# Performance work log

Measured on AMD Instinct MI355X. Metric: run time of the kernel, lower is better.

Reference implementation:

```python
import jax, jax.numpy as jnp
import numpy as np

B, NBAND, C, T = 2, 40, 64, 1500
NUM_CODE = 1024


def setup_inputs() -> dict:
    key = jax.random.key(0)
    k1, k2 = jax.random.split(key)
    x = jax.random.normal(k1, (B, NBAND, C, T), dtype=jnp.float32)
    # layer_idx == 0 init: unit-norm codes per band
    cb = jax.random.normal(k2, (NBAND, NUM_CODE, C), dtype=jnp.float32)
    eps = jnp.finfo(jnp.float32).eps
    cb = cb / jnp.sqrt(jnp.sum(cb * cb, axis=-1, keepdims=True) + eps)
    return {"x": x, "codebook": cb}


def reference(x, codebook):
    batch, nband, nchan, time = x.shape
    num_code = codebook.shape[1]
    # x.detach().permute(0,3,1,2).view(B*T, nband, nchan)
    xd = jax.lax.stop_gradient(x).transpose(0, 3, 1, 2).reshape(batch * time, nband, nchan)
    dist = (
        jnp.sum(xd * xd, axis=-1, keepdims=True)
        + jnp.sum(codebook * codebook, axis=-1)
        - 2.0 * jnp.einsum("nbc,bkc->nbk", xd, codebook)
    )
    min_idx = jnp.argmin(dist, axis=-1)  # [BT, nband]
    # per-band gather: quantized[n, b] = codebook[b, min_idx[n, b]]
    quantized = codebook[jnp.arange(nband)[None, :], min_idx]  # [BT, nband, nchan]
    # view(B, T, nband, nchan).permute(0,2,3,1)
    return quantized.reshape(batch, time, nband, nchan).transpose(0, 2, 3, 1)
```

## Files before the change

kernel.cpp:

```cpp
#include <hip/hip_runtime.h>


#define NBAND  40
#define CH     64
#define TT     1500
#define NCODE  1024
#define MT     128
#define NTILE  12
#define PAD    68
#define THRESH 1e-3f

typedef short v8s __attribute__((ext_vector_type(8)));
typedef float v4f __attribute__((ext_vector_type(4)));

#define CBF_USHORTS ((size_t)NBAND * 32 * 8 * 64 * 8)
#define CBF_BYTES   (CBF_USHORTS * 2)
#define WS_NEEDED   (CBF_BYTES + (size_t)NBAND * NCODE * 4)

__device__ __forceinline__ unsigned short f2bf(float f) {
    unsigned u = __float_as_uint(f);
    return (unsigned short)((u + 0x7FFFu + ((u >> 16) & 1u)) >> 16);
}
__device__ __forceinline__ float bf2f(unsigned short h) {
    return __uint_as_float(((unsigned)h) << 16);
}
__device__ __forceinline__ unsigned ford(float f) {
    unsigned u = __float_as_uint(f);
    return (u & 0x80000000u) ? ~u : (u | 0x80000000u);
}
__device__ __forceinline__ float finv(unsigned u) {
    return (u & 0x80000000u) ? __uint_as_float(u & 0x7FFFFFFFu) : __uint_as_float(~u);
}
__device__ __forceinline__ unsigned long long packsk(float f, unsigned k) {
    return ((unsigned long long)ford(f) << 32) | (unsigned long long)k;
}
__device__ __forceinline__ float med3f(float a, float b, float c) {
#if __has_builtin(__builtin_amdgcn_fmed3f)
    return __builtin_amdgcn_fmed3f(a, b, c);
#else
    return fminf(fmaxf(a, b), c);
#endif
}

typedef __attribute__((address_space(1))) const unsigned char* gas_p;
typedef __attribute__((address_space(3))) unsigned char*       las_p;
__device__ __forceinline__ void async_ld16(const void* g, void* l) {
    __builtin_amdgcn_global_load_lds((gas_p)g, (las_p)l, 16, 0, 0);
}

__global__ __launch_bounds__(256)
void vq_prep(const float* __restrict__ cb,
             unsigned short* __restrict__ CBF,
             float* __restrict__ C2) {
    const int id     = blockIdx.x;
    const int v      = id >> 3;
    const int band   = (id & 7) + 8 * (v % 5);
    const int gchunk = v / 5;
    const int g      = gchunk * 4 + (threadIdx.x >> 6);
    const int lane   = threadIdx.x & 63;
    const int col    = lane & 15;
    const int quad   = lane >> 4;

    float sq[2] = {0.f, 0.f};
    #pragma unroll
    for (int l = 0; l < 4; ++l) {
        const int ni = l >> 1, ks = l & 1;
        const int code = g * 32 + ni * 16 + col;
        const int c0   = ks * 32 + quad * 8;
        const float* src = cb + ((size_t)(band * NCODE + code)) * CH + c0;
        const float4 v0 = *(const float4*)src;
        const float4 v1 = *(const float4*)(src + 4);
        const float vv[8] = {v0.x, v0.y, v0.z, v0.w, v1.x, v1.y, v1.z, v1.w};
        union { unsigned short u[8]; v8s v; } hh, ll;
        #pragma unroll
        for (int j = 0; j < 8; ++j) {
            const unsigned short h = f2bf(vv[j]);
            hh.u[j] = h;
            ll.u[j] = f2bf(vv[j] - bf2f(h));
            sq[ni] = fmaf(vv[j], vv[j], sq[ni]);
        }
        const size_t gb = (size_t)(band * 32 + g) * 8;
        *(v8s*)&CBF[(gb + l)     * 512 + lane * 8] = hh.v;
        *(v8s*)&CBF[(gb + 4 + l) * 512 + lane * 8] = ll.v;
    }
    #pragma unroll
    for (int ni = 0; ni < 2; ++ni) {
        sq[ni] += __shfl_xor(sq[ni], 16);
        sq[ni] += __shfl_xor(sq[ni], 32);
    }
    if (quad == 0) {
        C2[band * NCODE + g * 32 + col]      = sq[0];
        C2[band * NCODE + g * 32 + 16 + col] = sq[1];
    }
}

__global__ __launch_bounds__(256, 3)
void vq_main(const float* __restrict__ x,
             const float* __restrict__ cb,
             const unsigned short* __restrict__ CBF,
             const float* __restrict__ C2f,
             float* __restrict__ out) {
    __shared__ alignas(16) unsigned char SMEM[MT * PAD * 2 * 2];
    __shared__ float c2_s[NCODE];
    __shared__ unsigned long long best_s[MT];
    __shared__ unsigned long long MB_s[MT * 2];
    __shared__ float MS_s[MT * 2];
    __shared__ unsigned amb_s[4];
    __shared__ float xrow_s[CH];

    const int id    = blockIdx.x;
    const int v     = id >> 3;
    const int band  = (id & 7) + 8 * (v % 5);
    const int tb    = v / 5;
    const int tile  = tb % NTILE;
    const int batch = tb / NTILE;
    const int t0    = tile * MT;

    const int tid   = threadIdx.x;
    const int wave  = tid >> 6;
    const int lane  = tid & 63;
    const int quad  = lane >> 4;
    const int col   = lane & 15;
    const int thalf = wave & 1;
    const int khalf = wave >> 1;

    if (tid < 4) amb_s[tid] = 0u;
    {
        const float* src = C2f + band * NCODE;
        #pragma unroll
        for (int i = 0; i < 4; ++i) c2_s[tid + 256 * i] = src[tid + 256 * i];
    }
    {
        unsigned short* XH_s = (unsigned short*)SMEM;
        unsigned short* XL_s = XH_s + MT * PAD;
        const int c = tid & 63;
        const int g = tid >> 6;
        const float* src = x + ((size_t)(batch * NBAND + band) * CH + c) * TT + t0;
        #pragma unroll
        for (int i = 0; i < 8; ++i) {
            const int t = (g + 4 * i) * 4;
            float4 v4 = make_float4(0.f, 0.f, 0.f, 0.f);
            if (t0 + t + 3 < TT) v4 = *(const float4*)(src + t);
            const float vv[4] = {v4.x, v4.y, v4.z, v4.w};
            #pragma unroll
            for (int j = 0; j < 4; ++j) {
                const unsigned short h = f2bf(vv[j]);
                XH_s[(t + j) * PAD + c] = h;
                XL_s[(t + j) * PAD + c] = f2bf(vv[j] - bf2f(h));
            }
        }
    }
    __syncthreads();

    v8s ah[4][2], al[4][2];
    {
        unsigned short* XH_s = (unsigned short*)SMEM;
        unsigned short* XL_s = XH_s + MT * PAD;
        #pragma unroll
        for (int mi = 0; mi < 4; ++mi)
            #pragma unroll
            for (int ks = 0; ks < 2; ++ks) {
                const int off = (thalf * 64 + mi * 16 + col) * PAD + ks * 32 + quad * 8;
                ah[mi][ks] = *(const v8s*)&XH_s[off];
                al[mi][ks] = *(const v8s*)&XL_s[off];
            }
    }
    __syncthreads();

    float m1[16], m2[16];
    int   id16[16];
    #pragma unroll
    for (int i = 0; i < 16; ++i) { m1[i] = 3.4028235e38f; m2[i] = 3.4028235e38f; id16[i] = 0x7fffffff; }

    unsigned short* LBUF = (unsigned short*)SMEM;
    const unsigned short* cbase = CBF + (size_t)(band * 32) * 4096 + (size_t)lane * 8;
    const int pbase = thalf * 4;

    auto stage_round = [&](int r, int b) {
        const int group = khalf * 16 + r;
        #pragma unroll
        for (int i = 0; i < 4; ++i) {
            const int p = pbase + i;
            async_ld16(cbase + (size_t)group * 4096 + p * 512,
                       LBUF + (size_t)b * 8192 + khalf * 4096 + p * 512);
        }
    };

    stage_round(0, 0);

    for (int r = 0; r < 16; ++r) {
        __syncthreads();
        if (r + 1 < 16) stage_round(r + 1, (r + 1) & 1);

        const unsigned short* lb = LBUF + (size_t)(r & 1) * 8192 + khalf * 4096 + lane * 8;
        #pragma unroll
        for (int ni = 0; ni < 2; ++ni) {
            v4f acc[4];
            #pragma unroll
            for (int mi = 0; mi < 4; ++mi) acc[mi] = (v4f){0.f, 0.f, 0.f, 0.f};
            #pragma unroll
            for (int ks = 0; ks < 2; ++ks) {
                const v8s bh = *(const v8s*)(lb + (ni * 2 + ks) * 512);
                #pragma unroll
                for (int mi = 0; mi < 4; ++mi)
                    acc[mi] = __builtin_amdgcn_mfma_f32_16x16x32_bf16(ah[mi][ks], bh, acc[mi], 0, 0, 0);
                #pragma unroll
                for (int mi = 0; mi < 4; ++mi)
                    acc[mi] = __builtin_amdgcn_mfma_f32_16x16x32_bf16(al[mi][ks], bh, acc[mi], 0, 0, 0);
                const v8s bl = *(const v8s*)(lb + (4 + ni * 2 + ks) * 512);
                #pragma unroll
                for (int mi = 0; mi < 4; ++mi)
                    acc[mi] = __builtin_amdgcn_mfma_f32_16x16x32_bf16(ah[mi][ks], bl, acc[mi], 0, 0, 0);
            }
            const int   kg  = khalf * 512 + r * 32 + ni * 16 + col;
            const float c2v = c2_s[kg];
            #pragma unroll
            for (int mi = 0; mi < 4; ++mi)
                #pragma unroll
                for (int rr = 0; rr < 4; ++rr) {
                    const int j = mi * 4 + rr;
                    const float s = fmaf(-2.f, acc[mi][rr], c2v);
                    m2[j] = med3f(s, m1[j], m2[j]);
                    const bool lt = s < m1[j];
                    m1[j]   = lt ? s : m1[j];
                    id16[j] = lt ? kg : id16[j];
                }
        }
    }

    #pragma unroll
    for (int j = 0; j < 16; ++j) {
        float b1 = m1[j], b2 = m2[j];
        int   bi = id16[j];
        #pragma unroll
        for (int d = 1; d < 16; d <<= 1) {
            const float o1 = __shfl_xor(b1, d);
            const float o2 = __shfl_xor(b2, d);
            const int   oi = __shfl_xor(bi, d);
            b2 = fminf(fminf(b2, o2), fmaxf(b1, o1));
            const bool take = (o1 < b1) || (o1 == b1 && oi < bi);
            b1 = take ? o1 : b1;
            bi = take ? oi : bi;
        }
        if (col == 0) {
            const int t = thalf * 64 + (j >> 2) * 16 + quad * 4 + (j & 3);
            MB_s[t * 2 + khalf] = packsk(b1, (unsigned)bi);
            MS_s[t * 2 + khalf] = b2;
        }
    }
    __syncthreads();

    if (tid < MT) {
        const unsigned long long b0 = MB_s[tid * 2];
        const unsigned long long b1 = MB_s[tid * 2 + 1];
        const unsigned long long bmin = (b0 < b1) ? b0 : b1;
        const unsigned long long bmax = (b0 < b1) ? b1 : b0;
        const float M1 = finv((unsigned)(bmin >> 32));
        const float M2 = fminf(fminf(MS_s[tid * 2], MS_s[tid * 2 + 1]), finv((unsigned)(bmax >> 32)));
        best_s[tid] = bmin;
        if ((M2 - M1) <= THRESH && t0 + tid < TT)
            atomicOr(&amb_s[tid >> 5], 1u << (tid & 31));
    }
    __syncthreads();

    for (int t = 0; t < MT; ++t) {
        if ((amb_s[t >> 5] >> (t & 31)) & 1u) {
            if (tid < CH) xrow_s[tid] = x[((size_t)(batch * NBAND + band) * CH + tid) * TT + t0 + t];
            if (tid == CH) best_s[t] = ~0ULL;
            __syncthreads();
            #pragma unroll
            for (int i = 0; i < 4; ++i) {
                const int k = tid * 4 + i;
                const float* crow = cb + ((size_t)(band * NCODE + k)) * CH;
                float dot = 0.f, c2e = 0.f;
                #pragma unroll 8
                for (int c = 0; c < CH; ++c) {
                    const float cv = crow[c];
                    dot = fmaf(cv, xrow_s[c], dot);
                    c2e = fmaf(cv, cv, c2e);
                }
                atomicMin(&best_s[t], packsk(fmaf(-2.f, dot, c2e), (unsigned)k));
            }
            __syncthreads();
        }
    }
    __syncthreads();

    {
        float* OT = (float*)SMEM;
        #pragma unroll
        for (int rr = 0; rr < MT; rr += 4) {
            const int row = rr + wave;
            const unsigned idx = (unsigned)(best_s[row] & 0xFFFFFFFFull) & (NCODE - 1);
            OT[row * 67 + lane] = cb[((size_t)(band * NCODE + idx)) * CH + lane];
        }
        __syncthreads();
        const int tloc  = tid & 127;
        const int chalf = tid >> 7;
        if (t0 + tloc < TT) {
            float* ob = out + ((size_t)(batch * NBAND + band) * CH) * TT + t0 + tloc;
            #pragma unroll
            for (int i = 0; i < 32; ++i) {
                const int c = chalf * 32 + i;
                ob[(size_t)c * TT] = OT[tloc * 67 + c];
            }
        }
    }
}

#define TN 128
#define KC 128
__global__ __launch_bounds__(256, 2)
void vq_fp32_kernel(const float* __restrict__ x,
                    const float* __restrict__ cb,
                    float* __restrict__ out) {
    __shared__ float XT_s[CH * TN];
    __shared__ float CBT_s[CH * KC];
    __shared__ float c2part[256];
    const int tile = blockIdx.x, band = blockIdx.y, batch = blockIdx.z;
    const int t0 = tile * TN;
    const int tid = threadIdx.x;
    const int tx = tid & 15, ty = tid >> 4;
    {
        const int c = tid >> 2, q = tid & 3;
        const float* src = x + ((size_t)(batch * NBAND + band) * CH + c) * TT + t0;
        #pragma unroll
        for (int i = 0; i < 8; ++i) {
            const int t = q * 32 + i * 4;
            float4 v = make_float4(0.f, 0.f, 0.f, 0.f);
            if (t0 + t < TT) v = *(const float4*)(src + t);
            *(float4*)&XT_s[c * TN + t] = v;
        }
    }
    float vmin[8]; int vidx[8];
    #pragma unroll
    for (int i = 0; i < 8; ++i) { vmin[i] = 3.4e38f; vidx[i] = 0x7fffffff; }
    for (int kc = 0; kc < NCODE; kc += KC) {
        __syncthreads();
        {
            const int k = tid >> 1, ch0 = (tid & 1) * 32;
            const float* src = cb + ((size_t)(band * NCODE + kc + k)) * CH + ch0;
            float s = 0.f;
            #pragma unroll
            for (int i = 0; i < 8; ++i) {
                const float4 v = *(const float4*)(src + i * 4);
                const int c0 = ch0 + i * 4;
                CBT_s[(c0 + 0) * KC + k] = v.x; CBT_s[(c0 + 1) * KC + k] = v.y;
                CBT_s[(c0 + 2) * KC + k] = v.z; CBT_s[(c0 + 3) * KC + k] = v.w;
                s = fmaf(v.x, v.x, s); s = fmaf(v.y, v.y, s);
                s = fmaf(v.z, v.z, s); s = fmaf(v.w, v.w, s);
            }
            c2part[tid] = s;
        }
        __syncthreads();
        float acc[8][8];
        #pragma unroll
        for (int ii = 0; ii < 8; ++ii)
            #pragma unroll
            for (int jj = 0; jj < 8; ++jj) acc[ii][jj] = 0.f;
        #pragma unroll 4
        for (int c = 0; c < CH; ++c) {
            const float4 xa0 = *(const float4*)&XT_s[c * TN + tx * 4];
            const float4 xa1 = *(const float4*)&XT_s[c * TN + 64 + tx * 4];
            const float4 cv0 = *(const float4*)&CBT_s[c * KC + ty * 4];
            const float4 cv1 = *(const float4*)&CBT_s[c * KC + 64 + ty * 4];
            const float xa[8] = {xa0.x, xa0.y, xa0.z, xa0.w, xa1.x, xa1.y, xa1.z, xa1.w};
            const float cv[8] = {cv0.x, cv0.y, cv0.z, cv0.w, cv1.x, cv1.y, cv1.z, cv1.w};
            #pragma unroll
            for (int ii = 0; ii < 8; ++ii)
                #pragma unroll
                for (int jj = 0; jj < 8; ++jj) acc[ii][jj] = fmaf(xa[ii], cv[jj], acc[ii][jj]);
        }
        #pragma unroll
        for (int jj = 0; jj < 8; ++jj) {
            const int kl = (jj < 4) ? (ty * 4 + jj) : (64 + ty * 4 + (jj - 4));
            const float c2v = c2part[2 * kl] + c2part[2 * kl + 1];
            const int kglob = kc + kl;
            #pragma unroll
            for (int ii = 0; ii < 8; ++ii) {
                const float score = fmaf(-2.f, acc[ii][jj], c2v);
                if (score < vmin[ii]) { vmin[ii] = score; vidx[ii] = kglob; }
            }
        }
    }
    __syncthreads();
    float* redv = XT_s;
    int* redi = (int*)(XT_s + TN * 16);
    int* idxs = (int*)(XT_s + TN * 32);
    #pragma unroll
    for (int ii = 0; ii < 8; ++ii) {
        const int t = (ii < 4) ? (tx * 4 + ii) : (64 + tx * 4 + (ii - 4));
        redv[t * 16 + ty] = vmin[ii];
        redi[t * 16 + ty] = vidx[ii];
    }
    __syncthreads();
    if (tid < TN) {
        float bv = redv[tid * 16]; int bi = redi[tid * 16];
        #pragma unroll
        for (int j = 1; j < 16; ++j) {
            const float v = redv[tid * 16 + j]; const int id = redi[tid * 16 + j];
            if (v < bv || (v == bv && id < bi)) { bv = v; bi = id; }
        }
        idxs[tid] = bi;
    }
    __syncthreads();
    {
        const int tloc = tid & 127, chalf = tid >> 7;
        if (t0 + tloc < TT) {
            const int idx = idxs[tloc];
            const float* crow = cb + ((size_t)(band * NCODE + idx)) * CH;
            float* ob = out + ((size_t)(batch * NBAND + band) * CH) * TT + t0 + tloc;
            #pragma unroll
            for (int i = 0; i < 32; ++i) {
                const int c = chalf * 32 + i;
                ob[(size_t)c * TT] = crow[c];
            }
        }
    }
}

extern "C" void kernel_launch(void* const* d_in, const int* in_sizes, int n_in,
                              void* d_out, int out_size, void* d_ws, size_t ws_size,
                              hipStream_t stream) {
    const float* x  = (const float*)d_in[0];
    const float* cb = (const float*)d_in[1];
    float* out = (float*)d_out;
    if (ws_size >= WS_NEEDED) {
        unsigned short* CBF = (unsigned short*)d_ws;
        float* C2 = (float*)((char*)d_ws + CBF_BYTES);
        vq_prep<<<dim3(8 * 5 * 8), dim3(256), 0, stream>>>(cb, CBF, C2);
        vq_main<<<dim3(8 * 5 * NTILE * 2), dim3(256), 0, stream>>>(x, cb, CBF, C2, out);
    } else {
        dim3 grid((TT + TN - 1) / TN, NBAND, 2);
        vq_fp32_kernel<<<grid, dim3(256), 0, stream>>>(x, cb, out);
    }
}
```

Measured before the change: 215.7 us.

## Split VQ search into x-prep, k-sliced partial argmin, and merge kernels

Replaces the monolithic per-tile kernel with four kernels. x is pre-split into bf16 hi/lo MFMA fragments in workspace. A k-sliced partial kernel launches 8x more blocks, each scanning 128 codes with smaller register and LDS footprint, and writes per-slice best and second-best scores. A merge kernel reduces the slices, runs the fp32 refinement for ambiguous rows and gathers the output. This is meant to raise parallelism and occupancy, at the cost of extra launches, workspace round trips and a strided x read in the prep kernel.

```diff
diff --git a/kernel.cpp b/kernel.cpp
--- a/kernel.cpp
+++ b/kernel.cpp
@@ -7,15 +7,22 @@
 #define NCODE  1024
 #define MT     128
 #define NTILE  12
-#define PAD    68
+#define NTG    48
 #define THRESH 1e-3f
 
 typedef short v8s __attribute__((ext_vector_type(8)));
 typedef float v4f __attribute__((ext_vector_type(4)));
 
-#define CBF_USHORTS ((size_t)NBAND * 32 * 8 * 64 * 8)
-#define CBF_BYTES   (CBF_USHORTS * 2)
-#define WS_NEEDED   (CBF_BYTES + (size_t)NBAND * NCODE * 4)
+#define CBF_BYTES  ((size_t)NBAND * 32 * 8 * 64 * 8 * 2)
+#define XF_OFF     CBF_BYTES
+#define XF_BYTES   ((size_t)2 * NBAND * NTG * 8 * 64 * 8 * 2)
+#define C2_OFF     (XF_OFF + XF_BYTES)
+#define C2_BYTES   ((size_t)NBAND * NCODE * 4)
+#define PB_OFF     (C2_OFF + C2_BYTES)
+#define PB_BYTES   ((size_t)2 * NBAND * 8 * 1536 * 8)
+#define PS_OFF     (PB_OFF + PB_BYTES)
+#define PS_BYTES   (PB_BYTES / 2)
+#define WS_NEEDED  (PS_OFF + PS_BYTES)
 
 __device__ __forceinline__ unsigned short f2bf(float f) {
     unsigned u = __float_as_uint(f);
@@ -49,9 +56,9 @@
 }
 
 __global__ __launch_bounds__(256)
-void vq_prep(const float* __restrict__ cb,
-             unsigned short* __restrict__ CBF,
-             float* __restrict__ C2) {
+void vq_prep_cb(const float* __restrict__ cb,
+                unsigned short* __restrict__ CBF,
+                float* __restrict__ C2) {
     const int id     = blockIdx.x;
     const int v      = id >> 3;
     const int band   = (id & 7) + 8 * (v % 5);
@@ -94,144 +101,137 @@
     }
 }
 
-__global__ __launch_bounds__(256, 3)
-void vq_main(const float* __restrict__ x,
-             const float* __restrict__ cb,
-             const unsigned short* __restrict__ CBF,
-             const float* __restrict__ C2f,
-             float* __restrict__ out) {
-    __shared__ alignas(16) unsigned char SMEM[MT * PAD * 2 * 2];
-    __shared__ float c2_s[NCODE];
-    __shared__ unsigned long long best_s[MT];
-    __shared__ unsigned long long MB_s[MT * 2];
-    __shared__ float MS_s[MT * 2];
-    __shared__ unsigned amb_s[4];
-    __shared__ float xrow_s[CH];
-
+__global__ __launch_bounds__(256)
+void vq_prep_x(const float* __restrict__ x,
+               unsigned short* __restrict__ XF) {
     const int id    = blockIdx.x;
     const int v     = id >> 3;
     const int band  = (id & 7) + 8 * (v % 5);
-    const int tb    = v / 5;
-    const int tile  = tb % NTILE;
-    const int batch = tb / NTILE;
-    const int t0    = tile * MT;
-
-    const int tid   = threadIdx.x;
-    const int wave  = tid >> 6;
-    const int lane  = tid & 63;
-    const int quad  = lane >> 4;
-    const int col   = lane & 15;
-    const int thalf = wave & 1;
-    const int khalf = wave >> 1;
-
-    if (tid < 4) amb_s[tid] = 0u;
+    const int u     = v / 5;
+    const int batch = u & 1;
+    const int chunk = u >> 1;
+    const int bb    = batch * NBAND + band;
+
+    const int wave = threadIdx.x >> 6;
+    const int lane = threadIdx.x & 63;
+    const int quad = lane >> 4;
+    const int col  = lane & 15;
+
+    #pragma unroll
+    for (int i = 0; i < 2; ++i) {
+        const int tg = chunk * 8 + wave * 2 + i;
+        #pragma unroll
+        for (int pp = 0; pp < 4; ++pp) {
+            const int mi = pp >> 1, ks = pp & 1;
+            const int t  = tg * 32 + mi * 16 + col;
+            union { unsigned short u[8]; v8s v; } hh, ll;
+            #pragma unroll
+            for (int j = 0; j < 8; ++j) {
+                const int c = ks * 32 + quad * 8 + j;
+                const float val = (t < TT) ? x[((size_t)bb * CH + c) * TT + t] : 0.f;
+                const unsigned short h = f2bf(val);
+                hh.u[j] = h;
+                ll.u[j] = f2bf(val - bf2f(h));
+            }
+            const size_t base = ((size_t)bb * NTG + tg) * 8;
+            *(v8s*)&XF[(base + pp)     * 512 + lane * 8] = hh.v;
+            *(v8s*)&XF[(base + 4 + pp) * 512 + lane * 8] = ll.v;
+        }
+    }
+}
+
+__global__ __launch_bounds__(256, 4)
+void vq_partial(const unsigned short* __restrict__ XF,
+                const unsigned short* __restrict__ CBF,
+                const float* __restrict__ C2f,
+                unsigned long long* __restrict__ PB,
+                float* __restrict__ PS) {
+    __shared__ alignas(16) unsigned short LBUF[4 * 8 * 512];
+
+    const int id     = blockIdx.x;
+    const int v      = id >> 3;
+    const int band   = (id & 7) + 8 * (v % 5);
+    const int u      = v / 5;
+    const int batch  = u & 1;
+    const int u2     = u >> 1;
+    const int tile   = u2 % NTILE;
+    const int kslice = u2 / NTILE;
+    const int bb     = batch * NBAND + band;
+
+    const int tid  = threadIdx.x;
+    const int wave = tid >> 6;
+    const int lane = tid & 63;
+    const int quad = lane >> 4;
+    const int col  = lane & 15;
+
     {
-        const float* src = C2f + band * NCODE;
-        #pragma unroll
-        for (int i = 0; i < 4; ++i) c2_s[tid + 256 * i] = src[tid + 256 * i];
-    }
+        const unsigned short* cbase =
+            CBF + ((size_t)(band * 32 + kslice * 4) * 8) * 512 + (size_t)lane * 8;
+        #pragma unroll
+        for (int i = 0; i < 8; ++i) {
+            const int fp = wave * 8 + i;
+            async_ld16(cbase + (size_t)fp * 512, LBUF + (size_t)fp * 512 + lane * 8);
+        }
+    }
+    v8s ah[2][2], al[2][2];
     {
-        unsigned short* XH_s = (unsigned short*)SMEM;
-        unsigned short* XL_s = XH_s + MT * PAD;
-        const int c = tid & 63;
-        const int g = tid >> 6;
-        const float* src = x + ((size_t)(batch * NBAND + band) * CH + c) * TT + t0;
-        #pragma unroll
-        for (int i = 0; i < 8; ++i) {
-            const int t = (g + 4 * i) * 4;
-            float4 v4 = make_float4(0.f, 0.f, 0.f, 0.f);
-            if (t0 + t + 3 < TT) v4 = *(const float4*)(src + t);
-            const float vv[4] = {v4.x, v4.y, v4.z, v4.w};
-            #pragma unroll
-            for (int j = 0; j < 4; ++j) {
-                const unsigned short h = f2bf(vv[j]);
-                XH_s[(t + j) * PAD + c] = h;
-                XL_s[(t + j) * PAD + c] = f2bf(vv[j] - bf2f(h));
-            }
-        }
-    }
-    __syncthreads();
-
-    v8s ah[4][2], al[4][2];
-    {
-        unsigned short* XH_s = (unsigned short*)SMEM;
-        unsigned short* XL_s = XH_s + MT * PAD;
-        #pragma unroll
-        for (int mi = 0; mi < 4; ++mi)
+        const int tg = tile * 4 + wave;
+        const unsigned short* xb =
+            XF + (((size_t)bb * NTG + tg) * 8) * 512 + (size_t)lane * 8;
+        #pragma unroll
+        for (int mi = 0; mi < 2; ++mi)
             #pragma unroll
             for (int ks = 0; ks < 2; ++ks) {
-                const int off = (thalf * 64 + mi * 16 + col) * PAD + ks * 32 + quad * 8;
-                ah[mi][ks] = *(const v8s*)&XH_s[off];
-                al[mi][ks] = *(const v8s*)&XL_s[off];
-            }
-    }
-    __syncthreads();
-
-    float m1[16], m2[16];
-    int   id16[16];
-    #pragma unroll
-    for (int i = 0; i < 16; ++i) { m1[i] = 3.4028235e38f; m2[i] = 3.4028235e38f; id16[i] = 0x7fffffff; }
-
-    unsigned short* LBUF = (unsigned short*)SMEM;
-    const unsigned short* cbase = CBF + (size_t)(band * 32) * 4096 + (size_t)lane * 8;
-    const int pbase = thalf * 4;
-
-    auto stage_round = [&](int r, int b) {
-        const int group = khalf * 16 + r;
-        #pragma unroll
-        for (int i = 0; i < 4; ++i) {
-            const int p = pbase + i;
-            async_ld16(cbase + (size_t)group * 4096 + p * 512,
-                       LBUF + (size_t)b * 8192 + khalf * 4096 + p * 512);
-        }
-    };
-
-    stage_round(0, 0);
-
-    for (int r = 0; r < 16; ++r) {
-        __syncthreads();
-        if (r + 1 < 16) stage_round(r + 1, (r + 1) & 1);
-
-        const unsigned short* lb = LBUF + (size_t)(r & 1) * 8192 + khalf * 4096 + lane * 8;
+                ah[mi][ks] = *(const v8s*)(xb + (mi * 2 + ks) * 512);
+                al[mi][ks] = *(const v8s*)(xb + (4 + mi * 2 + ks) * 512);
+            }
+    }
+    __syncthreads();
+
+    float m1[8], m2[8];
+    int   id8[8];
+    #pragma unroll
+    for (int i = 0; i < 8; ++i) { m1[i] = 3.4028235e38f; m2[i] = 3.4028235e38f; id8[i] = 0x7fffffff; }
+
+    #pragma unroll
+    for (int gi = 0; gi < 4; ++gi) {
+        const unsigned short* lb = LBUF + gi * 4096 + lane * 8;
         #pragma unroll
         for (int ni = 0; ni < 2; ++ni) {
-            v4f acc[4];
-            #pragma unroll
-            for (int mi = 0; mi < 4; ++mi) acc[mi] = (v4f){0.f, 0.f, 0.f, 0.f};
+            v4f acc[2];
+            acc[0] = (v4f){0.f, 0.f, 0.f, 0.f};
+            acc[1] = (v4f){0.f, 0.f, 0.f, 0.f};
             #pragma unroll
             for (int ks = 0; ks < 2; ++ks) {
                 const v8s bh = *(const v8s*)(lb + (ni * 2 + ks) * 512);
-                #pragma unroll
-                for (int mi = 0; mi < 4; ++mi)
-                    acc[mi] = __builtin_amdgcn_mfma_f32_16x16x32_bf16(ah[mi][ks], bh, acc[mi], 0, 0, 0);
-                #pragma unroll
-                for (int mi = 0; mi < 4; ++mi)
-                    acc[mi] = __builtin_amdgcn_mfma_f32_16x16x32_bf16(al[mi][ks], bh, acc[mi], 0, 0, 0);
+                acc[0] = __builtin_amdgcn_mfma_f32_16x16x32_bf16(ah[0][ks], bh, acc[0], 0, 0, 0);
+                acc[1] = __builtin_amdgcn_mfma_f32_16x16x32_bf16(ah[1][ks], bh, acc[1], 0, 0, 0);
+                acc[0] = __builtin_amdgcn_mfma_f32_16x16x32_bf16(al[0][ks], bh, acc[0], 0, 0, 0);
+                acc[1] = __builtin_amdgcn_mfma_f32_16x16x32_bf16(al[1][ks], bh, acc[1], 0, 0, 0);
                 const v8s bl = *(const v8s*)(lb + (4 + ni * 2 + ks) * 512);
-                #pragma unroll
-                for (int mi = 0; mi < 4; ++mi)
-                    acc[mi] = __builtin_amdgcn_mfma_f32_16x16x32_bf16(ah[mi][ks], bl, acc[mi], 0, 0, 0);
-            }
-            const int   kg  = khalf * 512 + r * 32 + ni * 16 + col;
-            const float c2v = c2_s[kg];
-            #pragma unroll
-            for (int mi = 0; mi < 4; ++mi)
+                acc[0] = __builtin_amdgcn_mfma_f32_16x16x32_bf16(ah[0][ks], bl, acc[0], 0, 0, 0);
+                acc[1] = __builtin_amdgcn_mfma_f32_16x16x32_bf16(ah[1][ks], bl, acc[1], 0, 0, 0);
+            }
+            const int   kg  = kslice * 128 + gi * 32 + ni * 16 + col;
+            const float c2v = C2f[band * NCODE + kg];
+            #pragma unroll
+            for (int mi = 0; mi < 2; ++mi)
                 #pragma unroll
                 for (int rr = 0; rr < 4; ++rr) {
                     const int j = mi * 4 + rr;
                     const float s = fmaf(-2.f, acc[mi][rr], c2v);
                     m2[j] = med3f(s, m1[j], m2[j]);
                     const bool lt = s < m1[j];
-                    m1[j]   = lt ? s : m1[j];
-                    id16[j] = lt ? kg : id16[j];
+                    m1[j]  = lt ? s : m1[j];
+                    id8[j] = lt ? kg : id8[j];
                 }
         }
     }
 
     #pragma unroll
-    for (int j = 0; j < 16; ++j) {
+    for (int j = 0; j < 8; ++j) {
         float b1 = m1[j], b2 = m2[j];
-        int   bi = id16[j];
+        int   bi = id8[j];
         #pragma unroll
         for (int d = 1; d < 16; d <<= 1) {
             const float o1 = __shfl_xor(b1, d);
@@ -243,29 +243,61 @@
             bi = take ? oi : bi;
         }
         if (col == 0) {
-            const int t = thalf * 64 + (j >> 2) * 16 + quad * 4 + (j & 3);
-            MB_s[t * 2 + khalf] = packsk(b1, (unsigned)bi);
-            MS_s[t * 2 + khalf] = b2;
-        }
-    }
+            const int tloc = wave * 32 + (j >> 2) * 16 + quad * 4 + (j & 3);
+            const size_t off = ((size_t)bb * 8 + kslice) * 1536 + tile * MT + tloc;
+            PB[off] = packsk(b1, (unsigned)bi);
+            PS[off] = b2;
+        }
+    }
+}
+
+__global__ __launch_bounds__(256)
+void vq_merge(const float* __restrict__ x,
+              const float* __restrict__ cb,
+              const unsigned long long* __restrict__ PB,
+              const float* __restrict__ PS,
+              float* __restrict__ out) {
+    __shared__ float OT[MT * 67];
+    __shared__ unsigned long long best_s[MT];
+    __shared__ unsigned amb_s[4];
+    __shared__ float xrow_s[CH];
+
+    const int id    = blockIdx.x;
+    const int v     = id >> 3;
+    const int band  = (id & 7) + 8 * (v % 5);
+    const int u     = v / 5;
+    const int batch = u & 1;
+    const int tile  = u >> 1;
+    const int bb    = batch * NBAND + band;
+    const int t0    = tile * MT;
+
+    const int tid = threadIdx.x;
+    if (tid < 4) amb_s[tid] = 0u;
     __syncthreads();
 
     if (tid < MT) {
-        const unsigned long long b0 = MB_s[tid * 2];
-        const unsigned long long b1 = MB_s[tid * 2 + 1];
-        const unsigned long long bmin = (b0 < b1) ? b0 : b1;
-        const unsigned long long bmax = (b0 < b1) ? b1 : b0;
-        const float M1 = finv((unsigned)(bmin >> 32));
-        const float M2 = fminf(fminf(MS_s[tid * 2], MS_s[tid * 2 + 1]), finv((unsigned)(bmax >> 32)));
+        const size_t base = (size_t)bb * 8 * 1536 + t0 + tid;
+        unsigned long long bmin = ~0ULL;
+        float s1 = 3.4028235e38f, s2 = 3.4028235e38f, psmin = 3.4028235e38f;
+        #pragma unroll
+        for (int ks = 0; ks < 8; ++ks) {
+            const unsigned long long b = PB[base + (size_t)ks * 1536];
+            const float sc = finv((unsigned)(b >> 32));
+            bmin = (b < bmin) ? b : bmin;
+            s2 = med3f(sc, s1, s2);
+            s1 = fminf(s1, sc);
+            psmin = fminf(psmin, PS[base + (size_t)ks * 1536]);
+        }
         best_s[tid] = bmin;
-        if ((M2 - M1) <= THRESH && t0 + tid < TT)
+        const float M2 = fminf(psmin, s2);
+        if ((M2 - s1) <= THRESH && t0 + tid < TT)
             atomicOr(&amb_s[tid >> 5], 1u << (tid & 31));
     }
     __syncthreads();
 
     for (int t = 0; t < MT; ++t) {
         if ((amb_s[t >> 5] >> (t & 31)) & 1u) {
-            if (tid < CH) xrow_s[tid] = x[((size_t)(batch * NBAND + band) * CH + tid) * TT + t0 + t];
+            if (tid < CH) xrow_s[tid] = x[((size_t)bb * CH + tid) * TT + t0 + t];
             if (tid == CH) best_s[t] = ~0ULL;
             __syncthreads();
             #pragma unroll
@@ -287,7 +319,8 @@
     __syncthreads();
 
     {
-        float* OT = (float*)SMEM;
+        const int wave = tid >> 6;
+        const int lane = tid & 63;
         #pragma unroll
         for (int rr = 0; rr < MT; rr += 4) {
             const int row = rr + wave;
@@ -298,7 +331,7 @@
         const int tloc  = tid & 127;
         const int chalf = tid >> 7;
         if (t0 + tloc < TT) {
-            float* ob = out + ((size_t)(batch * NBAND + band) * CH) * TT + t0 + tloc;
+            float* ob = out + ((size_t)bb * CH) * TT + t0 + tloc;
             #pragma unroll
             for (int i = 0; i < 32; ++i) {
                 const int c = chalf * 32 + i;
@@ -427,9 +460,14 @@
     float* out = (float*)d_out;
     if (ws_size >= WS_NEEDED) {
         unsigned short* CBF = (unsigned short*)d_ws;
-        float* C2 = (float*)((char*)d_ws + CBF_BYTES);
-        vq_prep<<<dim3(8 * 5 * 8), dim3(256), 0, stream>>>(cb, CBF, C2);
-        vq_main<<<dim3(8 * 5 * NTILE * 2), dim3(256), 0, stream>>>(x, cb, CBF, C2, out);
+        unsigned short* XF  = (unsigned short*)((char*)d_ws + XF_OFF);
+        float* C2           = (float*)((char*)d_ws + C2_OFF);
+        unsigned long long* PB = (unsigned long long*)((char*)d_ws + PB_OFF);
+        float* PS           = (float*)((char*)d_ws + PS_OFF);
+        vq_prep_cb<<<dim3(320), dim3(256), 0, stream>>>(cb, CBF, C2);
+        vq_prep_x <<<dim3(480), dim3(256), 0, stream>>>(x, XF);
+        vq_partial<<<dim3(7680), dim3(256), 0, stream>>>(XF, CBF, C2, PB, PS);
+        vq_merge  <<<dim3(960), dim3(256), 0, stream>>>(x, cb, PB, PS, out);
     } else {
         dim3 grid((TT + TN - 1) / TN, NBAND, 2);
         vq_fp32_kernel<<<grid, dim3(256), 0, stream>>>(x, cb, out);
```

Measured after the change: 255.9 us. +18.6%, slower.
